# Kernel optimization log

Hardware: AMD Instinct MI355X
Metric: run time of the kernel (lower is better)

## Reference

```python
import jax, jax.numpy as jnp
import numpy as np

OUT_H, OUT_W = 736, 240  # hardcoded interpolate target in the module


def resize_bilinear_ac(x, out_h, out_w):
    # bilinear, align_corners=True, NCHW
    B, C, H, W = x.shape
    def lin(n_in, n_out):
        pos = jnp.arange(n_out, dtype=jnp.float32) * (float(n_in - 1) / float(n_out - 1))
        i0 = jnp.floor(pos).astype(jnp.int32)
        i1 = jnp.minimum(i0 + 1, n_in - 1)
        f = pos - i0.astype(jnp.float32)
        return i0, i1, f
    hi0, hi1, hf = lin(H, out_h)
    xh = (x[:, :, hi0, :] * (1.0 - hf)[None, None, :, None]
          + x[:, :, hi1, :] * hf[None, None, :, None])
    wi0, wi1, wf = lin(W, out_w)
    return xh[..., wi0] * (1.0 - wf) + xh[..., wi1] * wf


def setup_inputs() -> dict:
    key = jax.random.key(0)
    x = jax.random.normal(key, (32, 7, 368, 120), dtype=jnp.float32)
    w = np.ones((6, 1, 1, 2), dtype=np.float32)
    w[:, :, :, 1] = -1.0  # fixed [1, -1] horizontal edge filter, depthwise
    return {"x": x, "dw_weight": jnp.asarray(w)}


def reference(x, dw_weight):
    C = x.shape[1]
    xi = resize_bilinear_ac(x, OUT_H, OUT_W)              # [B,C,736,240]
    lab = jnp.argmax(xi, axis=1)                          # [B,736,240]
    lab = jnp.transpose(lab, (0, 2, 1))                   # [B,240,736]
    oh = jax.nn.one_hot(lab, C, axis=1, dtype=jnp.float32)  # [B,C,240,736]

    # --- out1: depthwise [1,-1] diff with right pad of 0.5, relu, flipped argmax ---
    d = oh[:, :C - 1]                                     # drop background channel
    padded = jnp.pad(d, ((0, 0), (0, 0), (0, 0), (0, 1)), constant_values=0.5)
    w0 = dw_weight[:, 0, 0, 0][None, :, None, None]
    w1 = dw_weight[:, 0, 0, 1][None, :, None, None]
    edge = jax.nn.relu(padded[..., :-1] * w0 + padded[..., 1:] * w1)  # [B,C-1,240,736]
    t = jnp.transpose(edge, (0, 3, 2, 1))                 # [B,736,240,C-1]
    t = jnp.flip(t, axis=1)
    out1 = jnp.argmax(t, axis=1, keepdims=True)           # [B,1,240,C-1] int

    # --- out2: background channel summed over 8 bands of 30 rows ---
    xr = oh[:, -1]                                        # [B,240,736]
    B = xr.shape[0]
    out2 = xr.reshape(B, 8, 30, OUT_H).sum(axis=(2, 3)).reshape(B, 1, 8)
    return out1, out2
```

## Files before the change

### kernel.cpp

```cpp
#include <hip/hip_runtime.h>
#include <hip/hip_bf16.h>
#include <float.h>

#define BB 32
#define CC 7
#define IH 368
#define IW 120
#define OH 736
#define OW 240
#define NCH 92
#define CHROWS 8

#define OUT1_ELEMS (BB * OW * 6)

__global__ __launch_bounds__(256) void fused_label_edge_kernel(
    const float* __restrict__ x, unsigned long long* __restrict__ part) {
  int blk = blockIdx.x;
  int b = blk / NCH;
  int k = blk % NCH;
  int w = threadIdx.x;
  if (w >= OW) return;

  const float RH = (float)(367.0 / 735.0);
  const float RW = (float)(119.0 / 239.0);

  float pw = __fmul_rn((float)w, RW);
  int wi0 = (int)floorf(pw);
  int wi1 = min(wi0 + 1, IW - 1);
  float wf = __fsub_rn(pw, (float)wi0);
  float omwf = __fsub_rn(1.0f, wf);

  int h0 = k * CHROWS;
  const float* xb = x + (size_t)b * CC * IH * IW;

  float ph0 = __fmul_rn((float)h0, RH);
  int cur = (int)floorf(ph0);
  int rB = min(cur + 1, IH - 1);
  float tA0[CC], tA1[CC], tB0[CC], tB1[CC];
#pragma unroll
  for (int c = 0; c < CC; ++c) {
    const float* pa = xb + c * (IH * IW) + cur * IW;
    const float* pb = xb + c * (IH * IW) + rB * IW;
    tA0[c] = pa[wi0]; tA1[c] = pa[wi1];
    tB0[c] = pb[wi0]; tB1[c] = pb[wi1];
  }

  unsigned ep = 0;
  int c6 = 0;
  int prev = -1;

#define ROW_BODY(HL)                                                          \
  {                                                                           \
    int h = h0 + (HL);                                                        \
    float ph = __fmul_rn((float)h, RH);                                       \
    int hi0 = (int)floorf(ph);                                                \
    float hf = __fsub_rn(ph, (float)hi0);                                     \
    float omhf = __fsub_rn(1.0f, hf);                                         \
    if (hi0 != cur) {                               \
      cur = hi0;                                                              \
      int rN = min(cur + 1, IH - 1);                                          \
      _Pragma("unroll")                                                       \
      for (int c = 0; c < CC; ++c) {                                          \
        tA0[c] = tB0[c]; tA1[c] = tB1[c];                                     \
        const float* pp = xb + c * (IH * IW) + rN * IW;                       \
        tB0[c] = pp[wi0]; tB1[c] = pp[wi1];                                   \
      }                                                                       \
    }                                                                         \
    float best = -FLT_MAX;                                                    \
    int bc = 0;                                                               \
    _Pragma("unroll")                                                         \
    for (int c = 0; c < CC; ++c) {                                            \
      float va = __fadd_rn(__fmul_rn(tA0[c], omhf), __fmul_rn(tB0[c], hf));   \
      float vb = __fadd_rn(__fmul_rn(tA1[c], omhf), __fmul_rn(tB1[c], hf));   \
      float v  = __fadd_rn(__fmul_rn(va, omwf), __fmul_rn(vb, wf));           \
      if (v > best) { best = v; bc = c; }                                     \
    }                                                                         \
    if ((HL) < CHROWS) c6 += (bc == 6);                                       \
    if ((HL) > 0) {                                                           \
      int slot = prev * 5; \
      unsigned ins = (ep & ~(0x1fu << slot)) | ((unsigned)(HL) << slot);      \
      ep = (bc != prev) ? ins : ep;                                           \
    }                                                                         \
    prev = bc;                                                                \
  }

  ROW_BODY(0)
  ROW_BODY(1)
  ROW_BODY(2)
  ROW_BODY(3)
  ROW_BODY(4)
  ROW_BODY(5)
  ROW_BODY(6)
  ROW_BODY(7)
  if (k != NCH - 1) {
    ROW_BODY(8)
  }
#undef ROW_BODY

  unsigned long long u = (unsigned long long)(ep & 0x3FFFFFFFu) |
                         ((unsigned long long)(unsigned)c6 << 48);
  part[(size_t)(b * NCH + k) * OW + w] = u;
}

__global__ __launch_bounds__(256) void finalize_kernel(
    const unsigned long long* __restrict__ part, float* __restrict__ out) {
  int b = blockIdx.x;
  int w = threadIdx.x;

  __shared__ int cnt[256];

  int c6 = 0;
  if (w < OW) {
    int g0 = -1, g1 = -1, g2 = -1, g3 = -1, g4 = -1, g5 = -1;
    const unsigned long long* P = part + (size_t)b * NCH * OW + w;
#pragma unroll 4
    for (int kk = 0; kk < NCH; ++kk) {
      unsigned long long u = P[(size_t)kk * OW];
      int base = kk * CHROWS - 1;
      unsigned e = (unsigned)u;
      unsigned v;
      v = e & 0x1fu;          if (v) g0 = base + (int)v;
      v = (e >> 5) & 0x1fu;   if (v) g1 = base + (int)v;
      v = (e >> 10) & 0x1fu;  if (v) g2 = base + (int)v;
      v = (e >> 15) & 0x1fu;  if (v) g3 = base + (int)v;
      v = (e >> 20) & 0x1fu;  if (v) g4 = base + (int)v;
      v = (e >> 25) & 0x1fu;  if (v) g5 = base + (int)v;
      c6 += (int)((u >> 48) & 0xffu);
    }
    float* o1 = out + (size_t)b * (OW * 6) + w * 6;
    o1[0] = (g0 >= 0) ? (float)(735 - g0) : 0.0f;
    o1[1] = (g1 >= 0) ? (float)(735 - g1) : 0.0f;
    o1[2] = (g2 >= 0) ? (float)(735 - g2) : 0.0f;
    o1[3] = (g3 >= 0) ? (float)(735 - g3) : 0.0f;
    o1[4] = (g4 >= 0) ? (float)(735 - g4) : 0.0f;
    o1[5] = (g5 >= 0) ? (float)(735 - g5) : 0.0f;
  }

  cnt[threadIdx.x] = (w < OW) ? c6 : 0;
  __syncthreads();
  if (threadIdx.x < 8) {
    int s = 0;
#pragma unroll
    for (int i = 0; i < 30; ++i) s += cnt[threadIdx.x * 30 + i];
    out[OUT1_ELEMS + b * 8 + threadIdx.x] = (float)s;
  }
}

extern "C" void kernel_launch(void* const* d_in, const int* in_sizes, int n_in,
                              void* d_out, int out_size, void* d_ws, size_t ws_size,
                              hipStream_t stream) {
  const float* x = (const float*)d_in[0];
  float* out = (float*)d_out;
  unsigned long long* part = (unsigned long long*)d_ws;

  fused_label_edge_kernel<<<BB * NCH, 256, 0, stream>>>(x, part);
  finalize_kernel<<<BB, 256, 0, stream>>>(part, out);
}
```

Measured before the change: 109.6 us.

## Stage vertically interpolated rows in shared memory with float4 loads

The fused kernel now does the vertical interpolation cooperatively: all threads load input rows as float4 vectors, blend them vertically, and store the results in an LDS tile of 9 rows x 7 channels x 120 columns. After a barrier, each output column thread reads its two horizontal neighbours from LDS, interpolates, and runs the argmax and edge tracking. This swaps scattered per-thread scalar global gathers for coalesced vector loads and removes duplicate loads, since adjacent output columns share input columns. In exchange it adds a block barrier, about 30 KB of shared memory per block that may lower occupancy, and recomputes vertical blends for rows that could previously reuse cached values.

Result: faster. 104.0 us (-5.2%).

```diff
diff --git a/kernel.cpp b/kernel.cpp
--- a/kernel.cpp
+++ b/kernel.cpp
@@ -18,88 +18,91 @@
   int blk = blockIdx.x;
   int b = blk / NCH;
   int k = blk % NCH;
-  int w = threadIdx.x;
-  if (w >= OW) return;
+  int t = threadIdx.x;
 
   const float RH = (float)(367.0 / 735.0);
   const float RW = (float)(119.0 / 239.0);
 
-  float pw = __fmul_rn((float)w, RW);
-  int wi0 = (int)floorf(pw);
-  int wi1 = min(wi0 + 1, IW - 1);
-  float wf = __fsub_rn(pw, (float)wi0);
-  float omwf = __fsub_rn(1.0f, wf);
+  __shared__ float xh[9 * CC * IW];
 
   int h0 = k * CHROWS;
+  int nr = (k != NCH - 1) ? (CHROWS + 1) : CHROWS;
   const float* xb = x + (size_t)b * CC * IH * IW;
 
-  float ph0 = __fmul_rn((float)h0, RH);
-  int cur = (int)floorf(ph0);
-  int rB = min(cur + 1, IH - 1);
-  float tA0[CC], tA1[CC], tB0[CC], tB1[CC];
+  int nitems = nr * CC * (IW / 4);
+  for (int i = t; i < nitems; i += 256) {
+    int r = i / (CC * 30);
+    int rem = i - r * (CC * 30);
+    int c = rem / 30;
+    int p = rem - c * 30;
+    int wi = p * 4;
+    float ph = __fmul_rn((float)(h0 + r), RH);
+    int hi0 = (int)floorf(ph);
+    float hf = __fsub_rn(ph, (float)hi0);
+    float omhf = __fsub_rn(1.0f, hf);
+    int hi1 = min(hi0 + 1, IH - 1);
+    const float4 a = *(const float4*)(xb + ((size_t)c * IH + hi0) * IW + wi);
+    const float4 bb = *(const float4*)(xb + ((size_t)c * IH + hi1) * IW + wi);
+    float4 v;
+    v.x = __fadd_rn(__fmul_rn(a.x, omhf), __fmul_rn(bb.x, hf));
+    v.y = __fadd_rn(__fmul_rn(a.y, omhf), __fmul_rn(bb.y, hf));
+    v.z = __fadd_rn(__fmul_rn(a.z, omhf), __fmul_rn(bb.z, hf));
+    v.w = __fadd_rn(__fmul_rn(a.w, omhf), __fmul_rn(bb.w, hf));
+    *(float4*)&xh[(r * CC + c) * IW + wi] = v;
+  }
+  __syncthreads();
+
+  int w = t;
+  if (w < OW) {
+    float pw = __fmul_rn((float)w, RW);
+    int wi0 = (int)floorf(pw);
+    int wi1 = min(wi0 + 1, IW - 1);
+    float wf = __fsub_rn(pw, (float)wi0);
+    float omwf = __fsub_rn(1.0f, wf);
+
+    unsigned ep = 0;
+    int c6 = 0;
+    int prev = -1;
+
 #pragma unroll
-  for (int c = 0; c < CC; ++c) {
-    const float* pa = xb + c * (IH * IW) + cur * IW;
-    const float* pb = xb + c * (IH * IW) + rB * IW;
-    tA0[c] = pa[wi0]; tA1[c] = pa[wi1];
-    tB0[c] = pb[wi0]; tB1[c] = pb[wi1];
+    for (int r = 0; r < CHROWS; ++r) {
+      float best = -FLT_MAX;
+      int bc = 0;
+#pragma unroll
+      for (int c = 0; c < CC; ++c) {
+        float xl = xh[(r * CC + c) * IW + wi0];
+        float xr = xh[(r * CC + c) * IW + wi1];
+        float v = __fadd_rn(__fmul_rn(xl, omwf), __fmul_rn(xr, wf));
+        if (v > best) { best = v; bc = c; }
+      }
+      c6 += (bc == 6);
+      if (r > 0) {
+        int slot = prev * 5;
+        unsigned ins = (ep & ~(0x1fu << slot)) | ((unsigned)r << slot);
+        ep = (bc != prev) ? ins : ep;
+      }
+      prev = bc;
+    }
+    if (k != NCH - 1) {
+      float best = -FLT_MAX;
+      int bc = 0;
+#pragma unroll
+      for (int c = 0; c < CC; ++c) {
+        float xl = xh[(8 * CC + c) * IW + wi0];
+        float xr = xh[(8 * CC + c) * IW + wi1];
+        float v = __fadd_rn(__fmul_rn(xl, omwf), __fmul_rn(xr, wf));
+        if (v > best) { best = v; bc = c; }
+      }
+      if (bc != prev) {
+        int slot = prev * 5;
+        ep = (ep & ~(0x1fu << slot)) | (8u << slot);
+      }
+    }
+
+    unsigned long long u = (unsigned long long)(ep & 0x3FFFFFFFu) |
+                           ((unsigned long long)(unsigned)c6 << 48);
+    part[(size_t)(b * NCH + k) * OW + w] = u;
   }
-
-  unsigned ep = 0;
-  int c6 = 0;
-  int prev = -1;
-
-#define ROW_BODY(HL)                                                          \
-  {                                                                           \
-    int h = h0 + (HL);                                                        \
-    float ph = __fmul_rn((float)h, RH);                                       \
-    int hi0 = (int)floorf(ph);                                                \
-    float hf = __fsub_rn(ph, (float)hi0);                                     \
-    float omhf = __fsub_rn(1.0f, hf);                                         \
-    if (hi0 != cur) {                               \
-      cur = hi0;                                                              \
-      int rN = min(cur + 1, IH - 1);                                          \
-      _Pragma("unroll")                                                       \
-      for (int c = 0; c < CC; ++c) {                                          \
-        tA0[c] = tB0[c]; tA1[c] = tB1[c];                                     \
-        const float* pp = xb + c * (IH * IW) + rN * IW;                       \
-        tB0[c] = pp[wi0]; tB1[c] = pp[wi1];                                   \
-      }                                                                       \
-    }                                                                         \
-    float best = -FLT_MAX;                                                    \
-    int bc = 0;                                                               \
-    _Pragma("unroll")                                                         \
-    for (int c = 0; c < CC; ++c) {                                            \
-      float va = __fadd_rn(__fmul_rn(tA0[c], omhf), __fmul_rn(tB0[c], hf));   \
-      float vb = __fadd_rn(__fmul_rn(tA1[c], omhf), __fmul_rn(tB1[c], hf));   \
-      float v  = __fadd_rn(__fmul_rn(va, omwf), __fmul_rn(vb, wf));           \
-      if (v > best) { best = v; bc = c; }                                     \
-    }                                                                         \
-    if ((HL) < CHROWS) c6 += (bc == 6);                                       \
-    if ((HL) > 0) {                                                           \
-      int slot = prev * 5; \
-      unsigned ins = (ep & ~(0x1fu << slot)) | ((unsigned)(HL) << slot);      \
-      ep = (bc != prev) ? ins : ep;                                           \
-    }                                                                         \
-    prev = bc;                                                                \
-  }
-
-  ROW_BODY(0)
-  ROW_BODY(1)
-  ROW_BODY(2)
-  ROW_BODY(3)
-  ROW_BODY(4)
-  ROW_BODY(5)
-  ROW_BODY(6)
-  ROW_BODY(7)
-  if (k != NCH - 1) {
-    ROW_BODY(8)
-  }
-#undef ROW_BODY
-
-  unsigned long long u = (unsigned long long)(ep & 0x3FFFFFFFu) |
-                         ((unsigned long long)(unsigned)c6 << 48);
-  part[(size_t)(b * NCH + k) * OW + w] = u;
 }
 
 __global__ __launch_bounds__(256) void finalize_kernel(
```
